# Optimization experiments

Measured on AMD Instinct MI355X. Metric: run time of the kernel, lower is better.

The kernel has to match this reference:

```python
import jax, jax.numpy as jnp
import numpy as np

BN_EPS = 1e-5

def _conv1x1(x, w, b):
    # x: [B,C,H,W], w: [O,C], b: [O]
    return jnp.einsum('bchw,oc->bohw', x, w) + b[None, :, None, None]

def setup_inputs() -> dict:
    key = jax.random.key(0)
    ks = jax.random.split(key, 11)
    B, C, H, W = 4, 64, 80, 80
    s = 1.0 / np.sqrt(C)
    inp = {
        'x': jax.random.normal(ks[0], (B, C, H, W), jnp.float32),
        'w_theta': jax.random.normal(ks[1], (C, C), jnp.float32) * s,
        'b_theta': jax.random.normal(ks[2], (C,), jnp.float32) * s,
        'w_phi': jax.random.normal(ks[3], (C, C), jnp.float32) * s,
        'b_phi': jax.random.normal(ks[4], (C,), jnp.float32) * s,
        'w_g': jax.random.normal(ks[5], (C, C), jnp.float32) * s,
        'b_g': jax.random.normal(ks[6], (C,), jnp.float32) * s,
        'w_W': jax.random.normal(ks[7], (C, C), jnp.float32) * s,
        'b_W': jax.random.normal(ks[8], (C,), jnp.float32) * s,
        'gamma': jax.random.normal(ks[9], (C,), jnp.float32),
        'beta': jax.random.normal(ks[10], (C,), jnp.float32),
    }
    return inp

def reference(x, w_theta, b_theta, w_phi, b_phi, w_g, b_g, w_W, b_W, gamma, beta):
    B, C, H, W = x.shape
    N = H * W
    theta = _conv1x1(x, w_theta, b_theta).reshape(B, C, N).transpose(0, 2, 1)  # [B,N,C]
    phi = _conv1x1(x, w_phi, b_phi).reshape(B, C, N)                           # [B,C,N]
    g = _conv1x1(x, w_g, b_g).reshape(B, C, N).transpose(0, 2, 1)              # [B,N,C]
    f = jnp.einsum('bnc,bcm->bnm', theta, phi)                                  # [B,N,N]
    f_div_C = jax.nn.softmax(f, axis=-1)
    y = jnp.einsum('bnm,bmc->bnc', f_div_C, g)                                  # [B,N,C]
    y = y.transpose(0, 2, 1).reshape(B, C, H, W)
    Wy = _conv1x1(y, w_W, b_W)
    # BatchNorm2d in training mode: batch statistics over (B,H,W)
    mean = jnp.mean(Wy, axis=(0, 2, 3), keepdims=True)
    var = jnp.var(Wy, axis=(0, 2, 3), keepdims=True)
    bn = (Wy - mean) * jax.lax.rsqrt(var + BN_EPS)
    bn = bn * gamma[None, :, None, None] + beta[None, :, None, None]
    return bn + x
```

## Files before the change

### kernel.cpp

```cpp
#include <hip/hip_runtime.h>
#include <hip/hip_bf16.h>

#define NB 4
#define NC 64
#define NN 6400
#define NSEG 4
#define SEGK (NN / NSEG)
#define KVB 32
#define NIT (SEGK / KVB)
#define QBLK 128
#define BN_EPS 1e-5f
#define THR2 11.0f

#define BUFSZ 12288
#define PSOFF 24576
#define LDSSZ (2 * BUFSZ + 4 * 2560)

typedef __attribute__((ext_vector_type(4))) float f32x4;
typedef __attribute__((ext_vector_type(8))) __bf16 bf16x8;

static __device__ __forceinline__ f32x4 mfma_bf16(bf16x8 a, bf16x8 b, f32x4 c) {
    return __builtin_amdgcn_mfma_f32_16x16x32_bf16(a, b, c, 0, 0, 0);
}
static __device__ __forceinline__ float fexp2(float x) { return __builtin_amdgcn_exp2f(x); }
static __device__ __forceinline__ void gld16(const void* g, void* l) {
    __builtin_amdgcn_global_load_lds(
        (const __attribute__((address_space(1))) void*)g,
        (__attribute__((address_space(3))) void*)l, 16, 0, 0);
}
static __device__ __forceinline__ unsigned pk2(float a, float b) {
    unsigned ha = (unsigned)__builtin_bit_cast(unsigned short, __float2bfloat16(a));
    unsigned hb = (unsigned)__builtin_bit_cast(unsigned short, __float2bfloat16(b));
    return ha | (hb << 16);
}

__global__ __launch_bounds__(256) void k_qkv(
    const float* __restrict__ x,
    const float* __restrict__ w_th, const float* __restrict__ b_th,
    const float* __restrict__ w_ph, const float* __restrict__ b_ph,
    const float* __restrict__ w_g,  const float* __restrict__ b_g,
    __hip_bfloat16* __restrict__ Qh, __hip_bfloat16* __restrict__ Ql,
    __hip_bfloat16* __restrict__ Kh, __hip_bfloat16* __restrict__ Kl,
    __hip_bfloat16* __restrict__ Vt)
{
    __shared__ float xs[NC][68];
    __shared__ float ws[NC][65];

    const int bid = blockIdx.x;
    const int b   = bid / (NN / 64);
    const int n0  = (bid % (NN / 64)) * 64;
    const int t   = threadIdx.x;
    const int o   = t & 63;
    const int pr  = (t >> 6) * 16;

    {
        const int r  = t >> 2;
        const int cc = (t & 3) * 16;
        const float4* src = reinterpret_cast<const float4*>(x + (size_t)(b * NC + r) * NN + n0 + cc);
        float4* dst = reinterpret_cast<float4*>(&xs[r][cc]);
        dst[0] = src[0]; dst[1] = src[1]; dst[2] = src[2]; dst[3] = src[3];
    }

    const float* wptr[3] = { w_th, w_ph, w_g };
    const float* bptr[3] = { b_th, b_ph, b_g };

    #pragma unroll
    for (int cv = 0; cv < 3; ++cv) {
        __syncthreads();
        {
            const int oo = t & 63;
            const int cb = (t >> 6) * 16;
            const float4* src = reinterpret_cast<const float4*>(wptr[cv] + oo * NC + cb);
            float4 a0 = src[0], a1 = src[1], a2 = src[2], a3 = src[3];
            ws[cb +  0][oo] = a0.x; ws[cb +  1][oo] = a0.y; ws[cb +  2][oo] = a0.z; ws[cb +  3][oo] = a0.w;
            ws[cb +  4][oo] = a1.x; ws[cb +  5][oo] = a1.y; ws[cb +  6][oo] = a1.z; ws[cb +  7][oo] = a1.w;
            ws[cb +  8][oo] = a2.x; ws[cb +  9][oo] = a2.y; ws[cb + 10][oo] = a2.z; ws[cb + 11][oo] = a2.w;
            ws[cb + 12][oo] = a3.x; ws[cb + 13][oo] = a3.y; ws[cb + 14][oo] = a3.z; ws[cb + 15][oo] = a3.w;
        }
        __syncthreads();

        float acc[16];
        const float bb = bptr[cv][o];
        #pragma unroll
        for (int i = 0; i < 16; ++i) acc[i] = bb;

        #pragma unroll 8
        for (int c = 0; c < NC; ++c) {
            const float wv = ws[c][o];
            const float4* xr = reinterpret_cast<const float4*>(&xs[c][pr]);
            #pragma unroll
            for (int q = 0; q < 4; ++q) {
                const float4 xv = xr[q];
                acc[4*q + 0] = fmaf(wv, xv.x, acc[4*q + 0]);
                acc[4*q + 1] = fmaf(wv, xv.y, acc[4*q + 1]);
                acc[4*q + 2] = fmaf(wv, xv.z, acc[4*q + 2]);
                acc[4*q + 3] = fmaf(wv, xv.w, acc[4*q + 3]);
            }
        }

        if (cv < 2) {
            __hip_bfloat16* Hh = (cv == 0) ? Qh : Kh;
            __hip_bfloat16* Hl = (cv == 0) ? Ql : Kl;
            const float sc = (cv == 0) ? 1.44269504f : 1.0f;
            #pragma unroll
            for (int pp = 0; pp < 16; ++pp) {
                const float a = acc[pp] * sc;
                const __hip_bfloat16 h  = __float2bfloat16(a);
                const __hip_bfloat16 lo = __float2bfloat16(a - __bfloat162float(h));
                const size_t off = (size_t)(b * NN + n0 + pr + pp) * NC + o;
                Hh[off] = h;
                Hl[off] = lo;
            }
        } else {
            alignas(16) unsigned short gv[16];
            #pragma unroll
            for (int pp = 0; pp < 16; ++pp) {
                const __hip_bfloat16 h = __float2bfloat16(acc[pp]);
                gv[pp] = __builtin_bit_cast(unsigned short, h);
            }
            uint4* dst = reinterpret_cast<uint4*>(Vt + (size_t)(b * NC + o) * NN + n0 + pr);
            const uint4* srcv = reinterpret_cast<const uint4*>(gv);
            dst[0] = srcv[0];
            dst[1] = srcv[1];
        }
    }
}

__global__ __launch_bounds__(256, 3) void k_attn(
    const __hip_bfloat16* __restrict__ Qh, const __hip_bfloat16* __restrict__ Ql,
    const __hip_bfloat16* __restrict__ Kh, const __hip_bfloat16* __restrict__ Kl,
    const __hip_bfloat16* __restrict__ Vt,
    __hip_bfloat16* __restrict__ Op, float* __restrict__ Mm, float* __restrict__ Ll)
{
    __shared__ alignas(16) char lds[LDSSZ];

    const int phys = blockIdx.x;
    const int lid  = (phys & 7) * (NB * NSEG * (NN / QBLK) / 8) + (phys >> 3);
    const int grp  = lid / (NN / QBLK);
    const int qt   = lid % (NN / QBLK);
    const int b    = grp >> 2;
    const int seg  = grp & 3;
    const int q0   = qt * QBLK;

    const int t   = threadIdx.x;
    const int w   = t >> 6;
    const int l   = t & 63;
    const int l16 = l & 15;
    const int lg  = l >> 4;

    bf16x8 qh[2][2], ql[2][2];
    {
        const size_t qbase = (size_t)(b * NN + q0 + w * 32) * NC;
        #pragma unroll
        for (int qs = 0; qs < 2; ++qs) {
            const size_t ro = qbase + (size_t)(qs * 16 + l16) * NC + lg * 8;
            qh[qs][0] = *reinterpret_cast<const bf16x8*>(Qh + ro);
            qh[qs][1] = *reinterpret_cast<const bf16x8*>(Qh + ro + 32);
            ql[qs][0] = *reinterpret_cast<const bf16x8*>(Ql + ro);
            ql[qs][1] = *reinterpret_cast<const bf16x8*>(Ql + ro + 32);
        }
    }

    const __hip_bfloat16* khB = Kh + (size_t)(b * NN + seg * SEGK) * NC;
    const __hip_bfloat16* klB = Kl + (size_t)(b * NN + seg * SEGK) * NC;
    const __hip_bfloat16* vtB = Vt + (size_t)b * NC * NN + seg * SEGK;

    const int goffK = (w * 8 + (l >> 3)) * NC + (((l & 7) ^ (l >> 3)) * 8);
    const int goffV = (w * 16 + (l >> 2)) * NN + (((l & 3) ^ ((l >> 2) & 3)) * 8);

    const int swzK = l16 & 7;
    const int kA0  = l16 * 128 + ((lg ^ swzK) * 16);
    const int kA1  = l16 * 128 + (((lg + 4) ^ swzK) * 16);
    const int swzV = ((lg ^ (l16 & 3)) * 16);
    const int pW   = PSOFF + w * 2560 + l16 * 80 + lg * 8;
    const int pR   = PSOFF + w * 2560 + l16 * 80 + lg * 16;

    f32x4 accO[2][4];
    float mr[2], rsum[2];
    const f32x4 zero4 = {0.f, 0.f, 0.f, 0.f};
    #pragma unroll
    for (int qs = 0; qs < 2; ++qs) {
        mr[qs] = -3.0e38f; rsum[qs] = 0.f;
        #pragma unroll
        for (int c4 = 0; c4 < 4; ++c4) accO[qs][c4] = zero4;
    }

    auto STAGE = [&](int key0, char* bK) {
        gld16(khB + (size_t)key0 * NC + goffK, bK + w * 1024);
        gld16(klB + (size_t)key0 * NC + goffK, bK + 4096 + w * 1024);
        gld16(vtB + key0 + goffV,              bK + 8192 + w * 1024);
    };

    STAGE(0, lds);
    __syncthreads();
    int cur = 0;

    for (int it = 0; it < NIT; ++it) {
        char* bK = lds + cur * BUFSZ;
        if (it + 1 < NIT) STAGE((it + 1) * KVB, lds + (cur ^ 1) * BUFSZ);

        const bf16x8 kh0A = *reinterpret_cast<const bf16x8*>(bK + kA0);
        const bf16x8 kh1A = *reinterpret_cast<const bf16x8*>(bK + kA1);
        const bf16x8 kh0B = *reinterpret_cast<const bf16x8*>(bK + 2048 + kA0);
        const bf16x8 kh1B = *reinterpret_cast<const bf16x8*>(bK + 2048 + kA1);
        const bf16x8 kl0A = *reinterpret_cast<const bf16x8*>(bK + 4096 + kA0);
        const bf16x8 kl1A = *reinterpret_cast<const bf16x8*>(bK + 4096 + kA1);
        const bf16x8 kl0B = *reinterpret_cast<const bf16x8*>(bK + 4096 + 2048 + kA0);
        const bf16x8 kl1B = *reinterpret_cast<const bf16x8*>(bK + 4096 + 2048 + kA1);

        f32x4 sA[2], sB[2];
        #pragma unroll
        for (int qs = 0; qs < 2; ++qs) {
            f32x4 s = zero4;
            s = mfma_bf16(kh0A, qh[qs][0], s);
            s = mfma_bf16(kh1A, qh[qs][1], s);
            s = mfma_bf16(kl0A, qh[qs][0], s);
            s = mfma_bf16(kl1A, qh[qs][1], s);
            s = mfma_bf16(kh0A, ql[qs][0], s);
            s = mfma_bf16(kh1A, ql[qs][1], s);
            sA[qs] = s;
            f32x4 u = zero4;
            u = mfma_bf16(kh0B, qh[qs][0], u);
            u = mfma_bf16(kh1B, qh[qs][1], u);
            u = mfma_bf16(kl0B, qh[qs][0], u);
            u = mfma_bf16(kl1B, qh[qs][1], u);
            u = mfma_bf16(kh0B, ql[qs][0], u);
            u = mfma_bf16(kh1B, ql[qs][1], u);
            sB[qs] = u;
        }

        float pm[2];
        #pragma unroll
        for (int qs = 0; qs < 2; ++qs) {
            pm[qs] = fmaxf(fmaxf(fmaxf(sA[qs][0], sA[qs][1]), fmaxf(sA[qs][2], sA[qs][3])),
                           fmaxf(fmaxf(sB[qs][0], sB[qs][1]), fmaxf(sB[qs][2], sB[qs][3])));
        }
        const float dmax = fmaxf(pm[0] - mr[0], pm[1] - mr[1]);
        if (__any(dmax > THR2)) {
            float m0 = pm[0], m1 = pm[1];
            m0 = fmaxf(m0, __shfl_xor(m0, 16, 64));
            m0 = fmaxf(m0, __shfl_xor(m0, 32, 64));
            m1 = fmaxf(m1, __shfl_xor(m1, 16, 64));
            m1 = fmaxf(m1, __shfl_xor(m1, 32, 64));
            const float n0 = fmaxf(mr[0], m0), n1 = fmaxf(mr[1], m1);
            const float a0 = fexp2(mr[0] - n0), a1 = fexp2(mr[1] - n1);
            mr[0] = n0; mr[1] = n1;
            rsum[0] *= a0; rsum[1] *= a1;
            #pragma unroll
            for (int r = 0; r < 4; ++r) {
                const float b0 = __shfl(a0, lg * 4 + r, 64);
                const float b1 = __shfl(a1, lg * 4 + r, 64);
                #pragma unroll
                for (int c4 = 0; c4 < 4; ++c4) {
                    accO[0][c4][r] *= b0;
                    accO[1][c4][r] *= b1;
                }
            }
        }

        #pragma unroll
        for (int qs = 0; qs < 2; ++qs) {
            float pA[4], pB[4];
            #pragma unroll
            for (int r = 0; r < 4; ++r) {
                pA[r] = fexp2(sA[qs][r] - mr[qs]);
                pB[r] = fexp2(sB[qs][r] - mr[qs]);
            }
            rsum[qs] += (pA[0] + pA[1] + pA[2] + pA[3]) + (pB[0] + pB[1] + pB[2] + pB[3]);
            *reinterpret_cast<uint2*>(lds + pW + qs * 1280)      = make_uint2(pk2(pA[0], pA[1]), pk2(pA[2], pA[3]));
            *reinterpret_cast<uint2*>(lds + pW + qs * 1280 + 32) = make_uint2(pk2(pB[0], pB[1]), pk2(pB[2], pB[3]));
        }

        #pragma unroll
        for (int qs = 0; qs < 2; ++qs) {
            const bf16x8 pa = *reinterpret_cast<const bf16x8*>(lds + pR + qs * 1280);
            #pragma unroll
            for (int c4 = 0; c4 < 4; ++c4) {
                const bf16x8 vb = *reinterpret_cast<const bf16x8*>(bK + 8192 + (c4 * 16 + l16) * 64 + swzV);
                accO[qs][c4] = mfma_bf16(pa, vb, accO[qs][c4]);
            }
        }

        __syncthreads();
        cur ^= 1;
    }

    float rs[2] = { rsum[0], rsum[1] };
    #pragma unroll
    for (int qs = 0; qs < 2; ++qs) {
        rs[qs] += __shfl_xor(rs[qs], 16, 64);
        rs[qs] += __shfl_xor(rs[qs], 32, 64);
    }

    const size_t orow = (size_t)(seg * NB + b) * NN + q0 + w * 32;
    #pragma unroll
    for (int qs = 0; qs < 2; ++qs) {
        #pragma unroll
        for (int c4 = 0; c4 < 4; ++c4) {
            #pragma unroll
            for (int r = 0; r < 4; ++r) {
                Op[(orow + qs * 16 + lg * 4 + r) * NC + c4 * 16 + l16] = __float2bfloat16(accO[qs][c4][r]);
            }
        }
    }
    if (lg == 0) {
        #pragma unroll
        for (int qs = 0; qs < 2; ++qs) {
            Mm[orow + qs * 16 + l16] = mr[qs];
            Ll[orow + qs * 16 + l16] = rs[qs];
        }
    }
}

__global__ __launch_bounds__(256) void k_wconv(
    const __hip_bfloat16* __restrict__ Op, const float* __restrict__ Mm,
    const float* __restrict__ Ll, const float* __restrict__ w_W,
    const float* __restrict__ b_W, float* __restrict__ Wy,
    float* __restrict__ stats)
{
    __shared__ float ys[NC][68];
    __shared__ float ws[NC][65];

    const int bid = blockIdx.x;
    const int b   = bid / (NN / 64);
    const int n0  = (bid % (NN / 64)) * 64;
    const int t   = threadIdx.x;
    const int o   = t & 63;
    const int pr  = (t >> 6) * 16;

    {
        const int p  = t >> 2;
        const int cb = (t & 3) * 16;
        const size_t row = (size_t)b * NN + n0 + p;
        float m[NSEG], lv[NSEG];
        #pragma unroll
        for (int s = 0; s < NSEG; ++s) {
            m[s]  = Mm[(size_t)s * NB * NN + row];
            lv[s] = Ll[(size_t)s * NB * NN + row];
        }
        float mstar = m[0];
        #pragma unroll
        for (int s = 1; s < NSEG; ++s) mstar = fmaxf(mstar, m[s]);
        float acc16[16];
        #pragma unroll
        for (int j = 0; j < 16; ++j) acc16[j] = 0.f;
        float L = 0.f;
        #pragma unroll
        for (int s = 0; s < NSEG; ++s) {
            const float wsc = __builtin_amdgcn_exp2f(m[s] - mstar);
            L += wsc * lv[s];
            const bf16x8 a0 = *reinterpret_cast<const bf16x8*>(Op + ((size_t)s * NB * NN + row) * NC + cb);
            const bf16x8 a1 = *reinterpret_cast<const bf16x8*>(Op + ((size_t)s * NB * NN + row) * NC + cb + 8);
            #pragma unroll
            for (int j = 0; j < 8; ++j) {
                acc16[j]     = fmaf(wsc, (float)a0[j], acc16[j]);
                acc16[8 + j] = fmaf(wsc, (float)a1[j], acc16[8 + j]);
            }
        }
        const float inv = 1.0f / L;
        #pragma unroll
        for (int j = 0; j < 16; ++j) ys[cb + j][p] = acc16[j] * inv;
    }
    {
        const int oo = t & 63;
        const int cb = (t >> 6) * 16;
        const float4* src = reinterpret_cast<const float4*>(w_W + oo * NC + cb);
        float4 a0 = src[0], a1 = src[1], a2 = src[2], a3 = src[3];
        ws[cb +  0][oo] = a0.x; ws[cb +  1][oo] = a0.y; ws[cb +  2][oo] = a0.z; ws[cb +  3][oo] = a0.w;
        ws[cb +  4][oo] = a1.x; ws[cb +  5][oo] = a1.y; ws[cb +  6][oo] = a1.z; ws[cb +  7][oo] = a1.w;
        ws[cb +  8][oo] = a2.x; ws[cb +  9][oo] = a2.y; ws[cb + 10][oo] = a2.z; ws[cb + 11][oo] = a2.w;
        ws[cb + 12][oo] = a3.x; ws[cb + 13][oo] = a3.y; ws[cb + 14][oo] = a3.z; ws[cb + 15][oo] = a3.w;
    }
    __syncthreads();

    float acc[16];
    const float bb = b_W[o];
    #pragma unroll
    for (int i = 0; i < 16; ++i) acc[i] = bb;

    #pragma unroll 8
    for (int c = 0; c < NC; ++c) {
        const float wv = ws[c][o];
        const float4* xr = reinterpret_cast<const float4*>(&ys[c][pr]);
        #pragma unroll
        for (int q = 0; q < 4; ++q) {
            const float4 xv = xr[q];
            acc[4*q + 0] = fmaf(wv, xv.x, acc[4*q + 0]);
            acc[4*q + 1] = fmaf(wv, xv.y, acc[4*q + 1]);
            acc[4*q + 2] = fmaf(wv, xv.z, acc[4*q + 2]);
            acc[4*q + 3] = fmaf(wv, xv.w, acc[4*q + 3]);
        }
    }

    float s1 = 0.f, s2 = 0.f;
    #pragma unroll
    for (int i = 0; i < 16; ++i) { s1 += acc[i]; s2 += acc[i] * acc[i]; }

    float4* dst = reinterpret_cast<float4*>(Wy + (size_t)(b * NC + o) * NN + n0 + pr);
    const float4* av = reinterpret_cast<const float4*>(acc);
    dst[0] = av[0]; dst[1] = av[1]; dst[2] = av[2]; dst[3] = av[3];

    atomicAdd(&stats[o], s1);
    atomicAdd(&stats[NC + o], s2);
}

__global__ void k_zero(float* __restrict__ stats) {
    stats[threadIdx.x] = 0.f;
}

__global__ __launch_bounds__(256) void k_bn(
    const float* __restrict__ Wy, const float* __restrict__ x,
    const float* __restrict__ stats, const float* __restrict__ gamma,
    const float* __restrict__ beta, float* __restrict__ out)
{
    const int i = blockIdx.x * 256 + threadIdx.x;
    const int c = (i / (NN / 4)) % NC;
    const float n_inv = 1.0f / (float)(NB * NN);
    const float mean = stats[c] * n_inv;
    const float var  = stats[NC + c] * n_inv - mean * mean;
    const float rsq  = rsqrtf(var + BN_EPS);
    const float sc   = rsq * gamma[c];
    const float sh   = beta[c] - mean * sc;

    const float4 wv = reinterpret_cast<const float4*>(Wy)[i];
    const float4 xv = reinterpret_cast<const float4*>(x)[i];
    float4 ov;
    ov.x = wv.x * sc + sh + xv.x;
    ov.y = wv.y * sc + sh + xv.y;
    ov.z = wv.z * sc + sh + xv.z;
    ov.w = wv.w * sc + sh + xv.w;
    reinterpret_cast<float4*>(out)[i] = ov;
}

extern "C" void kernel_launch(void* const* d_in, const int* in_sizes, int n_in,
                              void* d_out, int out_size, void* d_ws, size_t ws_size,
                              hipStream_t stream)
{
    const float* x     = (const float*)d_in[0];
    const float* w_th  = (const float*)d_in[1];
    const float* b_th  = (const float*)d_in[2];
    const float* w_ph  = (const float*)d_in[3];
    const float* b_ph  = (const float*)d_in[4];
    const float* w_g   = (const float*)d_in[5];
    const float* b_g   = (const float*)d_in[6];
    const float* w_W   = (const float*)d_in[7];
    const float* b_W   = (const float*)d_in[8];
    const float* gamma = (const float*)d_in[9];
    const float* beta  = (const float*)d_in[10];
    float* out = (float*)d_out;

    char* p = (char*)d_ws;
    const size_t nbh = (size_t)NB * NN * NC * sizeof(__hip_bfloat16);
    __hip_bfloat16* Qh = (__hip_bfloat16*)p; p += nbh;
    __hip_bfloat16* Ql = (__hip_bfloat16*)p; p += nbh;
    __hip_bfloat16* Kh = (__hip_bfloat16*)p; p += nbh;
    __hip_bfloat16* Kl = (__hip_bfloat16*)p; p += nbh;
    __hip_bfloat16* Vt = (__hip_bfloat16*)p; p += nbh;
    __hip_bfloat16* Op = (__hip_bfloat16*)p; p += (size_t)NSEG * NB * NN * NC * sizeof(__hip_bfloat16);
    float* Mm    = (float*)p; p += (size_t)NSEG * NB * NN * sizeof(float);
    float* Ll    = (float*)p; p += (size_t)NSEG * NB * NN * sizeof(float);
    float* stats = (float*)p; p += 2 * NC * sizeof(float);
    float* Wy = (float*)d_ws;

    hipLaunchKernelGGL(k_qkv, dim3(NB * NN / 64), dim3(256), 0, stream,
                       x, w_th, b_th, w_ph, b_ph, w_g, b_g, Qh, Ql, Kh, Kl, Vt);
    hipLaunchKernelGGL(k_attn, dim3(NB * NSEG * (NN / QBLK)), dim3(256), 0, stream,
                       Qh, Ql, Kh, Kl, Vt, Op, Mm, Ll);
    hipLaunchKernelGGL(k_zero, dim3(1), dim3(2 * NC), 0, stream, stats);
    hipLaunchKernelGGL(k_wconv, dim3(NB * NN / 64), dim3(256), 0, stream,
                       Op, Mm, Ll, w_W, b_W, Wy, stats);
    hipLaunchKernelGGL(k_bn, dim3((NB * NC * NN / 4) / 256), dim3(256), 0, stream,
                       Wy, x, stats, gamma, beta, out);
}
```

Before: 271.3 us.

## Keep softmax probabilities in registers, split keys 8-way, halve conv tiles

```diff
diff --git a/kernel.cpp b/kernel.cpp
--- a/kernel.cpp
+++ b/kernel.cpp
@@ -4,19 +4,14 @@
 #define NB 4
 #define NC 64
 #define NN 6400
-#define NSEG 4
-#define SEGK (NN / NSEG)
 #define KVB 32
-#define NIT (SEGK / KVB)
 #define QBLK 128
 #define BN_EPS 1e-5f
 #define THR2 11.0f
 
 #define BUFSZ 12288
-#define PSOFF 24576
-#define LDSSZ (2 * BUFSZ + 4 * 2560)
-
-typedef __attribute__((ext_vector_type(4))) float f32x4;
+
+typedef __attribute__((ext_vector_type(4))) float  f32x4;
 typedef __attribute__((ext_vector_type(8))) __bf16 bf16x8;
 
 static __device__ __forceinline__ f32x4 mfma_bf16(bf16x8 a, bf16x8 b, f32x4 c) {
@@ -43,22 +38,22 @@
     __hip_bfloat16* __restrict__ Kh, __hip_bfloat16* __restrict__ Kl,
     __hip_bfloat16* __restrict__ Vt)
 {
-    __shared__ float xs[NC][68];
+    __shared__ float xs[NC][36];
     __shared__ float ws[NC][65];
 
     const int bid = blockIdx.x;
-    const int b   = bid / (NN / 64);
-    const int n0  = (bid % (NN / 64)) * 64;
+    const int b   = bid / (NN / 32);
+    const int n0  = (bid % (NN / 32)) * 32;
     const int t   = threadIdx.x;
     const int o   = t & 63;
-    const int pr  = (t >> 6) * 16;
+    const int pr  = (t >> 6) * 8;
 
     {
         const int r  = t >> 2;
-        const int cc = (t & 3) * 16;
+        const int cc = (t & 3) * 8;
         const float4* src = reinterpret_cast<const float4*>(x + (size_t)(b * NC + r) * NN + n0 + cc);
         float4* dst = reinterpret_cast<float4*>(&xs[r][cc]);
-        dst[0] = src[0]; dst[1] = src[1]; dst[2] = src[2]; dst[3] = src[3];
+        dst[0] = src[0]; dst[1] = src[1];
     }
 
     const float* wptr[3] = { w_th, w_ph, w_g };
@@ -79,17 +74,17 @@
         }
         __syncthreads();
 
-        float acc[16];
+        float acc[8];
         const float bb = bptr[cv][o];
         #pragma unroll
-        for (int i = 0; i < 16; ++i) acc[i] = bb;
+        for (int i = 0; i < 8; ++i) acc[i] = bb;
 
         #pragma unroll 8
         for (int c = 0; c < NC; ++c) {
             const float wv = ws[c][o];
             const float4* xr = reinterpret_cast<const float4*>(&xs[c][pr]);
             #pragma unroll
-            for (int q = 0; q < 4; ++q) {
+            for (int q = 0; q < 2; ++q) {
                 const float4 xv = xr[q];
                 acc[4*q + 0] = fmaf(wv, xv.x, acc[4*q + 0]);
                 acc[4*q + 1] = fmaf(wv, xv.y, acc[4*q + 1]);
@@ -103,7 +98,7 @@
             __hip_bfloat16* Hl = (cv == 0) ? Ql : Kl;
             const float sc = (cv == 0) ? 1.44269504f : 1.0f;
             #pragma unroll
-            for (int pp = 0; pp < 16; ++pp) {
+            for (int pp = 0; pp < 8; ++pp) {
                 const float a = acc[pp] * sc;
                 const __hip_bfloat16 h  = __float2bfloat16(a);
                 const __hip_bfloat16 lo = __float2bfloat16(a - __bfloat162float(h));
@@ -112,34 +107,36 @@
                 Hl[off] = lo;
             }
         } else {
-            alignas(16) unsigned short gv[16];
-            #pragma unroll
-            for (int pp = 0; pp < 16; ++pp) {
-                const __hip_bfloat16 h = __float2bfloat16(acc[pp]);
-                gv[pp] = __builtin_bit_cast(unsigned short, h);
-            }
-            uint4* dst = reinterpret_cast<uint4*>(Vt + (size_t)(b * NC + o) * NN + n0 + pr);
-            const uint4* srcv = reinterpret_cast<const uint4*>(gv);
-            dst[0] = srcv[0];
-            dst[1] = srcv[1];
-        }
-    }
-}
-
-__global__ __launch_bounds__(256, 3) void k_attn(
+            alignas(16) unsigned short gv[8];
+            #pragma unroll
+            for (int pp = 0; pp < 8; ++pp)
+                gv[pp] = __builtin_bit_cast(unsigned short, __float2bfloat16(acc[pp]));
+            *reinterpret_cast<uint4*>(Vt + (size_t)(b * NC + o) * NN + n0 + pr) =
+                *reinterpret_cast<const uint4*>(gv);
+        }
+    }
+}
+
+template<int NS>
+__global__ __launch_bounds__(256, 4) void k_attn(
     const __hip_bfloat16* __restrict__ Qh, const __hip_bfloat16* __restrict__ Ql,
     const __hip_bfloat16* __restrict__ Kh, const __hip_bfloat16* __restrict__ Kl,
     const __hip_bfloat16* __restrict__ Vt,
     __hip_bfloat16* __restrict__ Op, float* __restrict__ Mm, float* __restrict__ Ll)
 {
-    __shared__ alignas(16) char lds[LDSSZ];
+    constexpr int SEGK = NN / NS;
+    constexpr int NIT  = SEGK / KVB;
+    constexpr int NQT  = NN / QBLK;
+    constexpr int CPX  = NB * NS * NQT / 8;
+
+    __shared__ alignas(16) char lds[2 * BUFSZ];
 
     const int phys = blockIdx.x;
-    const int lid  = (phys & 7) * (NB * NSEG * (NN / QBLK) / 8) + (phys >> 3);
-    const int grp  = lid / (NN / QBLK);
-    const int qt   = lid % (NN / QBLK);
-    const int b    = grp >> 2;
-    const int seg  = grp & 3;
+    const int lid  = (phys & 7) * CPX + (phys >> 3);
+    const int grp  = lid / NQT;
+    const int qt   = lid % NQT;
+    const int b    = grp / NS;
+    const int seg  = grp % NS;
     const int q0   = qt * QBLK;
 
     const int t   = threadIdx.x;
@@ -171,9 +168,8 @@
     const int swzK = l16 & 7;
     const int kA0  = l16 * 128 + ((lg ^ swzK) * 16);
     const int kA1  = l16 * 128 + (((lg + 4) ^ swzK) * 16);
-    const int swzV = ((lg ^ (l16 & 3)) * 16);
-    const int pW   = PSOFF + w * 2560 + l16 * 80 + lg * 8;
-    const int pR   = PSOFF + w * 2560 + l16 * 80 + lg * 16;
+    const int slotA = (((lg >> 1) ^ (l16 & 3)) * 16) + (lg & 1) * 8;
+    const int slotB = (((2 + (lg >> 1)) ^ (l16 & 3)) * 16) + (lg & 1) * 8;
 
     f32x4 accO[2][4];
     float mr[2], rsum[2];
@@ -231,10 +227,9 @@
 
         float pm[2];
         #pragma unroll
-        for (int qs = 0; qs < 2; ++qs) {
+        for (int qs = 0; qs < 2; ++qs)
             pm[qs] = fmaxf(fmaxf(fmaxf(sA[qs][0], sA[qs][1]), fmaxf(sA[qs][2], sA[qs][3])),
                            fmaxf(fmaxf(sB[qs][0], sB[qs][1]), fmaxf(sB[qs][2], sB[qs][3])));
-        }
         const float dmax = fmaxf(pm[0] - mr[0], pm[1] - mr[1]);
         if (__any(dmax > THR2)) {
             float m0 = pm[0], m1 = pm[1];
@@ -258,6 +253,7 @@
             }
         }
 
+        bf16x8 pa8[2];
         #pragma unroll
         for (int qs = 0; qs < 2; ++qs) {
             float pA[4], pB[4];
@@ -267,18 +263,21 @@
                 pB[r] = fexp2(sB[qs][r] - mr[qs]);
             }
             rsum[qs] += (pA[0] + pA[1] + pA[2] + pA[3]) + (pB[0] + pB[1] + pB[2] + pB[3]);
-            *reinterpret_cast<uint2*>(lds + pW + qs * 1280)      = make_uint2(pk2(pA[0], pA[1]), pk2(pA[2], pA[3]));
-            *reinterpret_cast<uint2*>(lds + pW + qs * 1280 + 32) = make_uint2(pk2(pB[0], pB[1]), pk2(pB[2], pB[3]));
-        }
-
-        #pragma unroll
-        for (int qs = 0; qs < 2; ++qs) {
-            const bf16x8 pa = *reinterpret_cast<const bf16x8*>(lds + pR + qs * 1280);
-            #pragma unroll
-            for (int c4 = 0; c4 < 4; ++c4) {
-                const bf16x8 vb = *reinterpret_cast<const bf16x8*>(bK + 8192 + (c4 * 16 + l16) * 64 + swzV);
-                accO[qs][c4] = mfma_bf16(pa, vb, accO[qs][c4]);
-            }
+            uint4 pu;
+            pu.x = pk2(pA[0], pA[1]); pu.y = pk2(pA[2], pA[3]);
+            pu.z = pk2(pB[0], pB[1]); pu.w = pk2(pB[2], pB[3]);
+            pa8[qs] = __builtin_bit_cast(bf16x8, pu);
+        }
+
+        #pragma unroll
+        for (int c4 = 0; c4 < 4; ++c4) {
+            const int chb = (c4 * 16 + l16) * 64;
+            const uint2 va = *reinterpret_cast<const uint2*>(bK + 8192 + chb + slotA);
+            const uint2 vb = *reinterpret_cast<const uint2*>(bK + 8192 + chb + slotB);
+            uint4 vu; vu.x = va.x; vu.y = va.y; vu.z = vb.x; vu.w = vb.y;
+            const bf16x8 v8 = __builtin_bit_cast(bf16x8, vu);
+            accO[0][c4] = mfma_bf16(pa8[0], v8, accO[0][c4]);
+            accO[1][c4] = mfma_bf16(pa8[1], v8, accO[1][c4]);
         }
 
         __syncthreads();
@@ -299,7 +298,8 @@
         for (int c4 = 0; c4 < 4; ++c4) {
             #pragma unroll
             for (int r = 0; r < 4; ++r) {
-                Op[(orow + qs * 16 + lg * 4 + r) * NC + c4 * 16 + l16] = __float2bfloat16(accO[qs][c4][r]);
+                Op[(orow + qs * 16 + lg * 4 + r) * NC + c4 * 16 + l16] =
+                    __float2bfloat16(accO[qs][c4][r]);
             }
         }
     }
@@ -312,54 +312,52 @@
     }
 }
 
+template<int NS>
 __global__ __launch_bounds__(256) void k_wconv(
     const __hip_bfloat16* __restrict__ Op, const float* __restrict__ Mm,
     const float* __restrict__ Ll, const float* __restrict__ w_W,
     const float* __restrict__ b_W, float* __restrict__ Wy,
     float* __restrict__ stats)
 {
-    __shared__ float ys[NC][68];
+    __shared__ float ys[NC][36];
     __shared__ float ws[NC][65];
+    __shared__ float red[2][4][64];
 
     const int bid = blockIdx.x;
-    const int b   = bid / (NN / 64);
-    const int n0  = (bid % (NN / 64)) * 64;
+    const int b   = bid / (NN / 32);
+    const int n0  = (bid % (NN / 32)) * 32;
     const int t   = threadIdx.x;
     const int o   = t & 63;
-    const int pr  = (t >> 6) * 16;
+    const int pr  = (t >> 6) * 8;
 
     {
-        const int p  = t >> 2;
-        const int cb = (t & 3) * 16;
+        const int p  = t >> 3;
+        const int cb = (t & 7) * 8;
         const size_t row = (size_t)b * NN + n0 + p;
-        float m[NSEG], lv[NSEG];
-        #pragma unroll
-        for (int s = 0; s < NSEG; ++s) {
+        float m[NS], lv[NS];
+        #pragma unroll
+        for (int s = 0; s < NS; ++s) {
             m[s]  = Mm[(size_t)s * NB * NN + row];
             lv[s] = Ll[(size_t)s * NB * NN + row];
         }
         float mstar = m[0];
         #pragma unroll
-        for (int s = 1; s < NSEG; ++s) mstar = fmaxf(mstar, m[s]);
-        float acc16[16];
-        #pragma unroll
-        for (int j = 0; j < 16; ++j) acc16[j] = 0.f;
+        for (int s = 1; s < NS; ++s) mstar = fmaxf(mstar, m[s]);
+        float acc8[8];
+        #pragma unroll
+        for (int j = 0; j < 8; ++j) acc8[j] = 0.f;
         float L = 0.f;
         #pragma unroll
-        for (int s = 0; s < NSEG; ++s) {
-            const float wsc = __builtin_amdgcn_exp2f(m[s] - mstar);
+        for (int s = 0; s < NS; ++s) {
+            const float wsc = fexp2(m[s] - mstar);
             L += wsc * lv[s];
             const bf16x8 a0 = *reinterpret_cast<const bf16x8*>(Op + ((size_t)s * NB * NN + row) * NC + cb);
-            const bf16x8 a1 = *reinterpret_cast<const bf16x8*>(Op + ((size_t)s * NB * NN + row) * NC + cb + 8);
-            #pragma unroll
-            for (int j = 0; j < 8; ++j) {
-                acc16[j]     = fmaf(wsc, (float)a0[j], acc16[j]);
-                acc16[8 + j] = fmaf(wsc, (float)a1[j], acc16[8 + j]);
-            }
+            #pragma unroll
+            for (int j = 0; j < 8; ++j) acc8[j] = fmaf(wsc, (float)a0[j], acc8[j]);
         }
         const float inv = 1.0f / L;
         #pragma unroll
-        for (int j = 0; j < 16; ++j) ys[cb + j][p] = acc16[j] * inv;
+        for (int j = 0; j < 8; ++j) ys[cb + j][p] = acc8[j] * inv;
     }
     {
         const int oo = t & 63;
@@ -373,17 +371,17 @@
     }
     __syncthreads();
 
-    float acc[16];
+    float acc[8];
     const float bb = b_W[o];
     #pragma unroll
-    for (int i = 0; i < 16; ++i) acc[i] = bb;
+    for (int i = 0; i < 8; ++i) acc[i] = bb;
 
     #pragma unroll 8
     for (int c = 0; c < NC; ++c) {
         const float wv = ws[c][o];
         const float4* xr = reinterpret_cast<const float4*>(&ys[c][pr]);
         #pragma unroll
-        for (int q = 0; q < 4; ++q) {
+        for (int q = 0; q < 2; ++q) {
             const float4 xv = xr[q];
             acc[4*q + 0] = fmaf(wv, xv.x, acc[4*q + 0]);
             acc[4*q + 1] = fmaf(wv, xv.y, acc[4*q + 1]);
@@ -394,14 +392,21 @@
 
     float s1 = 0.f, s2 = 0.f;
     #pragma unroll
-    for (int i = 0; i < 16; ++i) { s1 += acc[i]; s2 += acc[i] * acc[i]; }
+    for (int i = 0; i < 8; ++i) { s1 += acc[i]; s2 += acc[i] * acc[i]; }
 
     float4* dst = reinterpret_cast<float4*>(Wy + (size_t)(b * NC + o) * NN + n0 + pr);
     const float4* av = reinterpret_cast<const float4*>(acc);
-    dst[0] = av[0]; dst[1] = av[1]; dst[2] = av[2]; dst[3] = av[3];
-
-    atomicAdd(&stats[o], s1);
-    atomicAdd(&stats[NC + o], s2);
+    dst[0] = av[0]; dst[1] = av[1];
+
+    red[0][t >> 6][o] = s1;
+    red[1][t >> 6][o] = s2;
+    __syncthreads();
+    if (t < 64) {
+        const float r1 = red[0][0][t] + red[0][1][t] + red[0][2][t] + red[0][3][t];
+        const float r2 = red[1][0][t] + red[1][1][t] + red[1][2][t] + red[1][3][t];
+        atomicAdd(&stats[t], r1);
+        atomicAdd(&stats[NC + t], r2);
+    }
 }
 
 __global__ void k_zero(float* __restrict__ stats) {
@@ -449,26 +454,36 @@
     const float* beta  = (const float*)d_in[10];
     float* out = (float*)d_out;
 
+    const size_t nbh = (size_t)NB * NN * NC * sizeof(__hip_bfloat16);
+    const size_t need8 = 5 * nbh + (size_t)8 * NB * NN * NC * 2 + (size_t)2 * 8 * NB * NN * 4 + 1024;
+    const int ns = (ws_size >= need8) ? 8 : 4;
+
     char* p = (char*)d_ws;
-    const size_t nbh = (size_t)NB * NN * NC * sizeof(__hip_bfloat16);
     __hip_bfloat16* Qh = (__hip_bfloat16*)p; p += nbh;
     __hip_bfloat16* Ql = (__hip_bfloat16*)p; p += nbh;
     __hip_bfloat16* Kh = (__hip_bfloat16*)p; p += nbh;
     __hip_bfloat16* Kl = (__hip_bfloat16*)p; p += nbh;
     __hip_bfloat16* Vt = (__hip_bfloat16*)p; p += nbh;
-    __hip_bfloat16* Op = (__hip_bfloat16*)p; p += (size_t)NSEG * NB * NN * NC * sizeof(__hip_bfloat16);
-    float* Mm    = (float*)p; p += (size_t)NSEG * NB * NN * sizeof(float);
-    float* Ll    = (float*)p; p += (size_t)NSEG * NB * NN * sizeof(float);
-    float* stats = (float*)p; p += 2 * NC * sizeof(float);
+    __hip_bfloat16* Op = (__hip_bfloat16*)p; p += (size_t)ns * NB * NN * NC * sizeof(__hip_bfloat16);
+    float* Mm    = (float*)p; p += (size_t)ns * NB * NN * sizeof(float);
+    float* Ll    = (float*)p; p += (size_t)ns * NB * NN * sizeof(float);
+    float* stats = (float*)p;
     float* Wy = (float*)d_ws;
 
-    hipLaunchKernelGGL(k_qkv, dim3(NB * NN / 64), dim3(256), 0, stream,
+    hipLaunchKernelGGL(k_zero, dim3(1), dim3(2 * NC), 0, stream, stats);
+    hipLaunchKernelGGL(k_qkv, dim3(NB * NN / 32), dim3(256), 0, stream,
                        x, w_th, b_th, w_ph, b_ph, w_g, b_g, Qh, Ql, Kh, Kl, Vt);
-    hipLaunchKernelGGL(k_attn, dim3(NB * NSEG * (NN / QBLK)), dim3(256), 0, stream,
-                       Qh, Ql, Kh, Kl, Vt, Op, Mm, Ll);
-    hipLaunchKernelGGL(k_zero, dim3(1), dim3(2 * NC), 0, stream, stats);
-    hipLaunchKernelGGL(k_wconv, dim3(NB * NN / 64), dim3(256), 0, stream,
-                       Op, Mm, Ll, w_W, b_W, Wy, stats);
+    if (ns == 8) {
+        hipLaunchKernelGGL(k_attn<8>, dim3(NB * 8 * (NN / QBLK)), dim3(256), 0, stream,
+                           Qh, Ql, Kh, Kl, Vt, Op, Mm, Ll);
+        hipLaunchKernelGGL(k_wconv<8>, dim3(NB * NN / 32), dim3(256), 0, stream,
+                           Op, Mm, Ll, w_W, b_W, Wy, stats);
+    } else {
+        hipLaunchKernelGGL(k_attn<4>, dim3(NB * 4 * (NN / QBLK)), dim3(256), 0, stream,
+                           Qh, Ql, Kh, Kl, Vt, Op, Mm, Ll);
+        hipLaunchKernelGGL(k_wconv<4>, dim3(NB * NN / 32), dim3(256), 0, stream,
+                           Op, Mm, Ll, w_W, b_W, Wy, stats);
+    }
     hipLaunchKernelGGL(k_bn, dim3((NB * NC * NN / 4) / 256), dim3(256), 0, stream,
                        Wy, x, stats, gamma, beta, out);
 }
```

After: 236.4 us. -12.9%, faster.
